# Kernel optimization log

Measured on AMD Instinct MI355X. Metric: run time of the kernel, lower is better.

## Reference

```python
import jax, jax.numpy as jnp
import numpy as np
import math

B, N, H, HEADS = 2, 4096, 256, 4
DH = H // HEADS
SCALE = math.sqrt(DH)


def setup_inputs() -> dict:
    key = jax.random.key(0)
    ks = jax.random.split(key, 8)
    h = jax.random.normal(ks[0], (B, N, H), dtype=jnp.float32)
    tau = jax.random.uniform(ks[1], (B, N), dtype=jnp.float32)  # trust scores in [0,1]
    adj_mask = jax.random.randint(ks[2], (N, N), 0, 2, dtype=jnp.int32)
    s = 0.02
    Wq = jax.random.normal(ks[3], (H, H), dtype=jnp.float32) * s
    Wk = jax.random.normal(ks[4], (H, H), dtype=jnp.float32) * s
    Wv = jax.random.normal(ks[5], (H, H), dtype=jnp.float32) * s
    Wo = jax.random.normal(ks[6], (H, H), dtype=jnp.float32) * s
    cw = jax.random.normal(ks[7], (HEADS,), dtype=jnp.float32) * s  # credibility_proj weight (num_heads,1) squeezed
    bq = jnp.zeros((H,), jnp.float32)
    bk = jnp.zeros((H,), jnp.float32)
    bv = jnp.zeros((H,), jnp.float32)
    bo = jnp.zeros((H,), jnp.float32)
    cb = jnp.zeros((HEADS,), jnp.float32)
    return {"h": h, "tau": tau, "adj_mask": adj_mask,
            "Wq": Wq, "bq": bq, "Wk": Wk, "bk": bk, "Wv": Wv, "bv": bv,
            "cw": cw, "cb": cb, "Wo": Wo, "bo": bo}


def reference(h, tau, adj_mask, Wq, bq, Wk, bk, Wv, bv, cw, cb, Wo, bo):
    # QKV projections -> (B, heads, N, head_dim)
    def proj(x, W, b):
        y = jnp.einsum('bnh,oh->bno', x, W) + b
        return y.reshape(B, N, HEADS, DH).transpose(0, 2, 1, 3)

    Q = proj(h, Wq, bq)
    K = proj(h, Wk, bk)
    V = proj(h, Wv, bv)

    scores = jnp.einsum('bhnd,bhmd->bhnm', Q, K) / SCALE  # (B,heads,N,N)
    # credibility bias: Linear(1 -> heads) applied to tau_i * tau_j
    tt = tau[:, :, None] * tau[:, None, :]                 # (B,N,N)
    cred = tt[:, None, :, :] * cw[None, :, None, None] + cb[None, :, None, None]
    scores = scores + cred
    # adjacency mask
    scores = jnp.where(adj_mask[None, None, :, :] == 0, -jnp.inf, scores)
    attention = jax.nn.softmax(scores, axis=-1)
    # dropout is identity in eval mode
    h_out = jnp.einsum('bhnm,bhmd->bhnd', attention, V)
    h_out = h_out.transpose(0, 2, 1, 3).reshape(B, N, H)
    h_out = jnp.einsum('bnh,oh->bno', h_out, Wo) + bo
    return h_out, attention.mean(axis=1)
```

## Files before the change

kernel.cpp:

```cpp
#include <hip/hip_runtime.h>

#define B_ 2
#define N_ 4096
#define H_ 256
#define HEADS_ 4
#define DH_ 64

typedef _Float16 f16;
typedef f16 f16x8 __attribute__((ext_vector_type(8)));
typedef f16 f16x4 __attribute__((ext_vector_type(4)));
typedef float f32x4 __attribute__((ext_vector_type(4)));


#define HOUT_OFF 2097152

__global__ __launch_bounds__(256) void cvt_kernel(
    const float* __restrict__ h, const float* __restrict__ Wq,
    const float* __restrict__ Wk, const float* __restrict__ Wv,
    const float* __restrict__ Wo, f16* __restrict__ ws) {
  int i = blockIdx.x * 256 + threadIdx.x;
  const int NH = 2097152;
  if (i < NH) {
    ws[i] = (f16)h[i];
  } else if (i < NH + 4 * 65536) {
    int j = i - NH;
    int sel = j >> 16;
    int k = j & 65535;
    const float* src = sel == 0 ? Wq : sel == 1 ? Wk : sel == 2 ? Wv : Wo;
    ws[i] = (f16)src[k];
  }
}

__global__ __launch_bounds__(256) void pack_adj_kernel(
    const int4* __restrict__ adj4, unsigned short* __restrict__ adjp) {
  int g = blockIdx.x * 256 + threadIdx.x;
  const int4* base = adj4 + (size_t)g * 4;
  unsigned m = 0;
#pragma unroll
  for (int t = 0; t < 4; ++t) {
    int4 v = base[t];
    m |= (unsigned)(v.x != 0) << (4 * t);
    m |= (unsigned)(v.y != 0) << (4 * t + 1);
    m |= (unsigned)(v.z != 0) << (4 * t + 2);
    m |= (unsigned)(v.w != 0) << (4 * t + 3);
  }
  adjp[g] = (unsigned short)m;
}

__global__ __launch_bounds__(256) void proj_kernel(
    const f16* __restrict__ hh, const f16* __restrict__ Wh,
    const float* __restrict__ bq, const float* __restrict__ bk,
    const float* __restrict__ bv, f16* __restrict__ Qh, f16* __restrict__ Kf,
    f16* __restrict__ Vf) {
  const int tid = threadIdx.x;
  const int lane = tid & 63, w = tid >> 6;
  const int q = lane >> 4, c = lane & 15;
  const int wsel = blockIdx.y >> 2, head = blockIdx.y & 3;
  const int m0 = blockIdx.x * 64 + w * 16;
  const f16* W = Wh + wsel * 65536;
  const int o0 = head * 64;

  f32x4 acc[4] = {};
  for (int k0 = 0; k0 < 256; k0 += 32) {
    f16x8 a = *(const f16x8*)(hh + (size_t)(m0 + c) * 256 + k0 + q * 8);
#pragma unroll
    for (int cg = 0; cg < 4; ++cg) {
      f16x8 bfr = *(const f16x8*)(W + (size_t)(o0 + cg * 16 + c) * 256 + k0 + q * 8);
      acc[cg] = __builtin_amdgcn_mfma_f32_16x16x32_f16(a, bfr, acc[cg], 0, 0, 0);
    }
  }
  const int b = m0 >> 12, n = m0 & 4095;
  const int bh2 = b * HEADS_ + head;
  if (wsel == 2) {
    const int jt = n >> 6;
    f16* vbase = Vf + (((size_t)bh2 * 64 + jt) * 8) * 512;
#pragma unroll
    for (int cg = 0; cg < 4; ++cg) {
      float bb = bv[o0 + cg * 16 + c];
#pragma unroll
      for (int r = 0; r < 4; ++r) {
        int jj = w * 16 + q * 4 + r;
        vbase[(size_t)(((jj >> 5) * 4 + cg) * 512) + ((jj >> 3) & 3) * 128 +
              c * 8 + (jj & 7)] = (f16)(acc[cg][r] + bb);
      }
    }
  } else if (wsel == 1) {
    const int t = n >> 4;
    f16* kbase = Kf + (((size_t)bh2 * 256 + t) * 2) * 512;
#pragma unroll
    for (int cg = 0; cg < 4; ++cg) {
      float bb = bk[o0 + cg * 16 + c];
      const int half = cg >> 1;
      const int qf = ((cg & 1) * 16 + c) >> 3;
      f16* kb2 = kbase + half * 512 + qf * 128 + (c & 7);
#pragma unroll
      for (int r = 0; r < 4; ++r) kb2[(q * 4 + r) * 8] = (f16)(acc[cg][r] + bb);
    }
  } else {
#pragma unroll
    for (int cg = 0; cg < 4; ++cg) {
      int dh = cg * 16 + c;
      float bb = bq[o0 + dh];
#pragma unroll
      for (int r = 0; r < 4; ++r)
        Qh[((size_t)bh2 * N_ + n + q * 4 + r) * DH_ + dh] =
            (f16)((acc[cg][r] + bb) * 0.125f);
    }
  }
}

#define TSH 80
#define PTILE (16 * TSH)

__global__ __launch_bounds__(256, 1) void attn_sum_kernel(
    const f16* __restrict__ Qh, const f16* __restrict__ Kf,
    const f16* __restrict__ Vf, const float* __restrict__ tau,
    const uint2* __restrict__ adjb, const float* __restrict__ cw,
    f16* __restrict__ Oh, float* __restrict__ rsum_ws) {
  __shared__ f16 ptile[8 * PTILE];
  __shared__ float ocomb[4][1024];
  __shared__ float lred[4][32];
  const int gid = blockIdx.x;
  const int bh = gid & 7;
  const int b = bh >> 2, h = bh & 3;
  const int i0 = (gid >> 3) * 32;
  const int tid = threadIdx.x;
  const int lane = tid & 63, jq = tid >> 6;
  const int q = lane >> 4, c = lane & 15;

  f16x8 a0[2], a1[2];
  float tau_i[2][4];
#pragma unroll
  for (int ig = 0; ig < 2; ++ig) {
    const f16* Qbase = Qh + ((size_t)bh * N_ + i0 + ig * 16 + c) * DH_;
    a0[ig] = *(const f16x8*)(Qbase + q * 8);
    a1[ig] = *(const f16x8*)(Qbase + 32 + q * 8);
#pragma unroll
    for (int r = 0; r < 4; ++r)
      tau_i[ig][r] = tau[b * N_ + i0 + ig * 16 + q * 4 + r];
  }
  const float cw_h = cw[h];
  const f16* Kfb = Kf + (size_t)bh * 262144 + lane * 8;
  const f16* Vfb = Vf + (size_t)bh * 262144 + lane * 8;
  const float* taub = tau + b * N_;
  const int jbase = jq * 1024;

  float lsum[2][4] = {};
  f32x4 oacc[2][4] = {};
  f16* myp0 = ptile + (jq * 2) * PTILE;
  f16* myp1 = myp0 + PTILE;

#pragma unroll 1
  for (int it = 0; it < 16; ++it) {
    const int j0 = jbase + it * 64;
    f16x8 kf[8];
    {
      const f16* kt = Kfb + (size_t)(j0 >> 4) * 1024;
#pragma unroll
      for (int f = 0; f < 8; ++f) kf[f] = *(const f16x8*)(kt + f * 512);
    }
    float tj[4];
#pragma unroll
    for (int cg = 0; cg < 4; ++cg) tj[cg] = taub[j0 + cg * 16 + c];

    {
      uint2 aw[4];
#pragma unroll
      for (int r = 0; r < 4; ++r)
        aw[r] = adjb[(size_t)(i0 + q * 4 + r) * 64 + (j0 >> 6)];
#pragma unroll
      for (int cg = 0; cg < 4; ++cg) {
        f32x4 s = {};
        s = __builtin_amdgcn_mfma_f32_16x16x32_f16(a0[0], kf[2 * cg], s, 0, 0, 0);
        s = __builtin_amdgcn_mfma_f32_16x16x32_f16(a1[0], kf[2 * cg + 1], s, 0, 0, 0);
        const float credj = cw_h * tj[cg];
        const unsigned shift = (cg & 1) * 16 + c;
#pragma unroll
        for (int r = 0; r < 4; ++r) {
          unsigned mword = (cg < 2) ? aw[r].x : aw[r].y;
          float e = __expf(s[r] + credj * tau_i[0][r]);
          e = ((mword >> shift) & 1) ? e : 0.f;
          lsum[0][r] += e;
          myp0[(q * 4 + r) * TSH + cg * 16 + c] = (f16)e;
        }
      }
    }
    f16x8 vf[8];
    {
      const f16* vt = Vfb + (size_t)(j0 >> 6) * 4096;
#pragma unroll
      for (int f = 0; f < 8; ++f) vf[f] = *(const f16x8*)(vt + f * 512);
    }
    {
      uint2 aw[4];
#pragma unroll
      for (int r = 0; r < 4; ++r)
        aw[r] = adjb[(size_t)(i0 + 16 + q * 4 + r) * 64 + (j0 >> 6)];
#pragma unroll
      for (int cg = 0; cg < 4; ++cg) {
        f32x4 s = {};
        s = __builtin_amdgcn_mfma_f32_16x16x32_f16(a0[1], kf[2 * cg], s, 0, 0, 0);
        s = __builtin_amdgcn_mfma_f32_16x16x32_f16(a1[1], kf[2 * cg + 1], s, 0, 0, 0);
        const float credj = cw_h * tj[cg];
        const unsigned shift = (cg & 1) * 16 + c;
#pragma unroll
        for (int r = 0; r < 4; ++r) {
          unsigned mword = (cg < 2) ? aw[r].x : aw[r].y;
          float e = __expf(s[r] + credj * tau_i[1][r]);
          e = ((mword >> shift) & 1) ? e : 0.f;
          lsum[1][r] += e;
          myp1[(q * 4 + r) * TSH + cg * 16 + c] = (f16)e;
        }
      }
    }
#pragma unroll
    for (int ig = 0; ig < 2; ++ig) {
      const f16* myp = ig ? myp1 : myp0;
#pragma unroll
      for (int ks = 0; ks < 2; ++ks) {
        f16x8 pa = *(const f16x8*)(myp + c * TSH + ks * 32 + q * 8);
#pragma unroll
        for (int cg = 0; cg < 4; ++cg)
          oacc[ig][cg] = __builtin_amdgcn_mfma_f32_16x16x32_f16(
              pa, vf[ks * 4 + cg], oacc[ig][cg], 0, 0, 0);
      }
    }
  }

#pragma unroll
  for (int ig = 0; ig < 2; ++ig) {
#pragma unroll
    for (int r = 0; r < 4; ++r) {
      float v = lsum[ig][r];
      v += __shfl_xor(v, 1);
      v += __shfl_xor(v, 2);
      v += __shfl_xor(v, 4);
      v += __shfl_xor(v, 8);
      lsum[ig][r] = v;
    }
  }
  if (c == 0) {
#pragma unroll
    for (int ig = 0; ig < 2; ++ig)
#pragma unroll
      for (int r = 0; r < 4; ++r) lred[jq][ig * 16 + q * 4 + r] = lsum[ig][r];
  }
  __syncthreads();

#pragma unroll
  for (int ig = 0; ig < 2; ++ig) {
    float linv[4];
#pragma unroll
    for (int r = 0; r < 4; ++r) {
      int row = ig * 16 + q * 4 + r;
      linv[r] = 1.0f / (lred[0][row] + lred[1][row] + lred[2][row] +
                        lred[3][row]);
    }
    if (jq == 0 && c == 0) {
#pragma unroll
      for (int r = 0; r < 4; ++r)
        rsum_ws[bh * N_ + i0 + ig * 16 + q * 4 + r] = linv[r];
    }
    if (jq != 0) {
#pragma unroll
      for (int cg = 0; cg < 4; ++cg)
#pragma unroll
        for (int r = 0; r < 4; ++r)
          ocomb[jq][(cg * 4 + r) * 64 + lane] = oacc[ig][cg][r];
    }
    __syncthreads();
    if (jq == 0) {
#pragma unroll
      for (int cg = 0; cg < 4; ++cg)
#pragma unroll
        for (int r = 0; r < 4; ++r) {
          float v = oacc[ig][cg][r];
#pragma unroll
          for (int jj = 1; jj < 4; ++jj)
            v += ocomb[jj][(cg * 4 + r) * 64 + lane];
          Oh[((size_t)(b * N_) + i0 + ig * 16 + q * 4 + r) * H_ + h * 64 +
             cg * 16 + c] = (f16)(v * linv[r]);
        }
    }
    __syncthreads();
  }
}

__global__ __launch_bounds__(256, 1) void attn_mean_kernel(
    const f16* __restrict__ Qh, const f16* __restrict__ Kf,
    const float* __restrict__ tau, const uint2* __restrict__ adjb,
    const float* __restrict__ cw, const float* __restrict__ linv_ws,
    float* __restrict__ out) {
  const int gid = blockIdx.x;
  const int b = gid & 1;
  const int jq = (gid >> 1) & 3;
  const int i0 = (gid >> 3) * 16;
  const int tid = threadIdx.x;
  const int lane = tid & 63, w = tid >> 6;
  const int q = lane >> 4, c = lane & 15;

  float li[4][4];
  float cwh[4];
#pragma unroll
  for (int h = 0; h < 4; ++h) {
    cwh[h] = cw[h];
#pragma unroll
    for (int r = 0; r < 4; ++r)
      li[h][r] = linv_ws[(b * 4 + h) * N_ + i0 + q * 4 + r] * 0.25f;
  }
  float tau_i[4];
#pragma unroll
  for (int r = 0; r < 4; ++r) tau_i[r] = tau[b * N_ + i0 + q * 4 + r];
  const float* taub = tau + b * N_;
  const f16* KfB = Kf + (size_t)(b * 4) * 262144 + lane * 8;
  const f16* QB = Qh + ((size_t)(b * 4) * N_ + i0 + c) * DH_;

  f16x8 kf2[2][8];
  f16x8 qa2[2][2];
  {
    const int j0 = jq * 1024 + w * 64;
    const f16* kt = KfB + (size_t)(j0 >> 4) * 1024;
#pragma unroll
    for (int f = 0; f < 8; ++f) kf2[0][f] = *(const f16x8*)(kt + f * 512);
    qa2[0][0] = *(const f16x8*)(QB + q * 8);
    qa2[0][1] = *(const f16x8*)(QB + 32 + q * 8);
  }

#pragma unroll 1
  for (int it = 0; it < 4; ++it) {
    const int j0 = jq * 1024 + (it * 4 + w) * 64;
    uint2 aw[4];
#pragma unroll
    for (int r = 0; r < 4; ++r)
      aw[r] = adjb[(size_t)(i0 + q * 4 + r) * 64 + (j0 >> 6)];
    float tj[4];
#pragma unroll
    for (int cg = 0; cg < 4; ++cg) tj[cg] = taub[j0 + cg * 16 + c];

    f32x4 macc[4] = {};
#pragma unroll
    for (int h = 0; h < 4; ++h) {
      const int cur = h & 1, nx = cur ^ 1;
      {
        const int hn = (h + 1) & 3;
        const int itn = (h < 3) ? it : (it < 3 ? it + 1 : it);
        const int j0n = jq * 1024 + (itn * 4 + w) * 64;
        const f16* ktn = KfB + (size_t)hn * 262144 + (size_t)(j0n >> 4) * 1024;
#pragma unroll
        for (int f = 0; f < 8; ++f) kf2[nx][f] = *(const f16x8*)(ktn + f * 512);
        const f16* qn = QB + (size_t)hn * 262144;
        qa2[nx][0] = *(const f16x8*)(qn + q * 8);
        qa2[nx][1] = *(const f16x8*)(qn + 32 + q * 8);
      }
#pragma unroll
      for (int cg = 0; cg < 4; ++cg) {
        f32x4 s = {};
        s = __builtin_amdgcn_mfma_f32_16x16x32_f16(qa2[cur][0], kf2[cur][2 * cg],
                                                   s, 0, 0, 0);
        s = __builtin_amdgcn_mfma_f32_16x16x32_f16(qa2[cur][1],
                                                   kf2[cur][2 * cg + 1], s, 0, 0, 0);
        const float credj = cwh[h] * tj[cg];
        const unsigned shift = (cg & 1) * 16 + c;
#pragma unroll
        for (int r = 0; r < 4; ++r) {
          unsigned mword = (cg < 2) ? aw[r].x : aw[r].y;
          float e = __expf(s[r] + credj * tau_i[r]);
          float lw = ((mword >> shift) & 1) ? li[h][r] : 0.f;
          macc[cg][r] += e * lw;
        }
      }
    }
#pragma unroll
    for (int cg = 0; cg < 4; ++cg)
#pragma unroll
      for (int r = 0; r < 4; ++r)
        out[((size_t)(b * N_) + i0 + q * 4 + r) * N_ + j0 + cg * 16 + c] =
            macc[cg][r];
  }
}

__global__ __launch_bounds__(256) void oproj_kernel(
    const f16* __restrict__ Oh, const f16* __restrict__ Woh,
    const float* __restrict__ bo, float* __restrict__ out) {
  const int tid = threadIdx.x, lane = tid & 63, w = tid >> 6;
  const int q = lane >> 4, c = lane & 15;
  const int m0 = blockIdx.x * 64 + w * 16;
  const int o0 = blockIdx.y * 64;
  f32x4 acc[4] = {};
  for (int k0 = 0; k0 < 256; k0 += 32) {
    f16x8 a = *(const f16x8*)(Oh + (size_t)(m0 + c) * 256 + k0 + q * 8);
#pragma unroll
    for (int cg = 0; cg < 4; ++cg) {
      f16x8 bfr = *(const f16x8*)(Woh + (size_t)(o0 + cg * 16 + c) * 256 + k0 + q * 8);
      acc[cg] = __builtin_amdgcn_mfma_f32_16x16x32_f16(a, bfr, acc[cg], 0, 0, 0);
    }
  }
#pragma unroll
  for (int cg = 0; cg < 4; ++cg) {
    float bb = bo[o0 + cg * 16 + c];
#pragma unroll
    for (int r = 0; r < 4; ++r)
      out[(size_t)(m0 + q * 4 + r) * 256 + o0 + cg * 16 + c] = acc[cg][r] + bb;
  }
}

extern "C" void kernel_launch(void* const* d_in, const int* in_sizes, int n_in,
                              void* d_out, int out_size, void* d_ws,
                              size_t ws_size, hipStream_t stream) {
  const float* h   = (const float*)d_in[0];
  const float* tau = (const float*)d_in[1];
  const int*   adj = (const int*)d_in[2];
  const float* Wq  = (const float*)d_in[3];
  const float* bq  = (const float*)d_in[4];
  const float* Wk  = (const float*)d_in[5];
  const float* bk  = (const float*)d_in[6];
  const float* Wv  = (const float*)d_in[7];
  const float* bv  = (const float*)d_in[8];
  const float* cw  = (const float*)d_in[9];
  const float* Wo  = (const float*)d_in[11];
  const float* bo  = (const float*)d_in[12];
  float* out = (float*)d_out;

  f16* ws   = (f16*)d_ws;
  f16* h_h  = ws;
  f16* W_h  = ws + 2097152;
  f16* Wo_h = W_h + 3 * 65536;
  f16* Q_h  = ws + 2359296;
  f16* K_f  = ws + 4456448;
  f16* V_f  = ws + 6553600;
  f16* O_h  = ws + 8650752;
  unsigned long long* adjb = (unsigned long long*)(ws + 10747904);
  float* rsum_ws = (float*)ws;

  pack_adj_kernel<<<dim3(4096), dim3(256), 0, stream>>>(
      (const int4*)adj, (unsigned short*)adjb);
  cvt_kernel<<<dim3(9216), dim3(256), 0, stream>>>(h, Wq, Wk, Wv, Wo, ws);
  proj_kernel<<<dim3(128, 12), dim3(256), 0, stream>>>(h_h, W_h, bq, bk, bv, Q_h,
                                                       K_f, V_f);
  attn_sum_kernel<<<dim3(1024), dim3(256), 0, stream>>>(
      Q_h, K_f, V_f, tau, (const uint2*)adjb, cw, O_h, rsum_ws);
  attn_mean_kernel<<<dim3(2048), dim3(256), 0, stream>>>(
      Q_h, K_f, tau, (const uint2*)adjb, cw, rsum_ws, out + HOUT_OFF);
  oproj_kernel<<<dim3(128, 4), dim3(256), 0, stream>>>(O_h, Wo_h, bo, out);
}
```

Baseline: 386.7 us.

## Software-pipeline K loads across iterations and store P tile as fp32 in LDS

Loads the first half of the next iteration's K fragments and tau values early so they overlap the current iteration's compute. V fragment loads are split into two halves, and the loop is unrolled by 2. The P tile in LDS is now fp32 with a 68-float stride and is converted to f16 on read. The same LDS buffer is reused for the cross-wave output combine, replacing the separate ocomb array. In exchange it raises register pressure and doubles the LDS bytes per P element, adding conversion instructions.

```diff
diff --git a/kernel.cpp b/kernel.cpp
--- a/kernel.cpp
+++ b/kernel.cpp
@@ -109,16 +109,15 @@
   }
 }
 
-#define TSH 80
-#define PTILE (16 * TSH)
+#define TS 68
+#define WTILE (16 * TS)
 
 __global__ __launch_bounds__(256, 1) void attn_sum_kernel(
     const f16* __restrict__ Qh, const f16* __restrict__ Kf,
     const f16* __restrict__ Vf, const float* __restrict__ tau,
     const uint2* __restrict__ adjb, const float* __restrict__ cw,
     f16* __restrict__ Oh, float* __restrict__ rsum_ws) {
-  __shared__ f16 ptile[8 * PTILE];
-  __shared__ float ocomb[4][1024];
+  __shared__ float lds[8 * WTILE];
   __shared__ float lred[4][32];
   const int gid = blockIdx.x;
   const int bh = gid & 7;
@@ -147,21 +146,29 @@
 
   float lsum[2][4] = {};
   f32x4 oacc[2][4] = {};
-  f16* myp0 = ptile + (jq * 2) * PTILE;
-  f16* myp1 = myp0 + PTILE;
-
-#pragma unroll 1
+  float* myp0 = lds + (jq * 2) * WTILE;
+  float* myp1 = myp0 + WTILE;
+
+  f16x8 kfA[2][4];
+  float tjA[2][4];
+  {
+    const f16* kt = Kfb + (size_t)(jbase >> 4) * 1024;
+#pragma unroll
+    for (int f = 0; f < 4; ++f) kfA[0][f] = *(const f16x8*)(kt + f * 512);
+#pragma unroll
+    for (int cg = 0; cg < 4; ++cg) tjA[0][cg] = taub[jbase + cg * 16 + c];
+  }
+
+#pragma unroll 2
   for (int it = 0; it < 16; ++it) {
+    const int cur = it & 1, nx = cur ^ 1;
     const int j0 = jbase + it * 64;
-    f16x8 kf[8];
+    f16x8 kfB[4];
     {
       const f16* kt = Kfb + (size_t)(j0 >> 4) * 1024;
 #pragma unroll
-      for (int f = 0; f < 8; ++f) kf[f] = *(const f16x8*)(kt + f * 512);
-    }
-    float tj[4];
-#pragma unroll
-    for (int cg = 0; cg < 4; ++cg) tj[cg] = taub[j0 + cg * 16 + c];
+      for (int f = 0; f < 4; ++f) kfB[f] = *(const f16x8*)(kt + (4 + f) * 512);
+    }
 
     {
       uint2 aw[4];
@@ -171,9 +178,11 @@
 #pragma unroll
       for (int cg = 0; cg < 4; ++cg) {
         f32x4 s = {};
-        s = __builtin_amdgcn_mfma_f32_16x16x32_f16(a0[0], kf[2 * cg], s, 0, 0, 0);
-        s = __builtin_amdgcn_mfma_f32_16x16x32_f16(a1[0], kf[2 * cg + 1], s, 0, 0, 0);
-        const float credj = cw_h * tj[cg];
+        f16x8 k0 = (cg < 2) ? kfA[cur][2 * cg] : kfB[2 * (cg - 2)];
+        f16x8 k1 = (cg < 2) ? kfA[cur][2 * cg + 1] : kfB[2 * (cg - 2) + 1];
+        s = __builtin_amdgcn_mfma_f32_16x16x32_f16(a0[0], k0, s, 0, 0, 0);
+        s = __builtin_amdgcn_mfma_f32_16x16x32_f16(a1[0], k1, s, 0, 0, 0);
+        const float credj = cw_h * tjA[cur][cg];
         const unsigned shift = (cg & 1) * 16 + c;
 #pragma unroll
         for (int r = 0; r < 4; ++r) {
@@ -181,16 +190,27 @@
           float e = __expf(s[r] + credj * tau_i[0][r]);
           e = ((mword >> shift) & 1) ? e : 0.f;
           lsum[0][r] += e;
-          myp0[(q * 4 + r) * TSH + cg * 16 + c] = (f16)e;
+          myp0[(q * 4 + r) * TS + cg * 16 + c] = e;
         }
       }
     }
-    f16x8 vf[8];
+
+    {
+      const int itn = (it < 15) ? it + 1 : it;
+      const int jn = jbase + itn * 64;
+      const f16* kt = Kfb + (size_t)(jn >> 4) * 1024;
+#pragma unroll
+      for (int f = 0; f < 4; ++f) kfA[nx][f] = *(const f16x8*)(kt + f * 512);
+#pragma unroll
+      for (int cg = 0; cg < 4; ++cg) tjA[nx][cg] = taub[jn + cg * 16 + c];
+    }
+    f16x8 vf0[4];
     {
       const f16* vt = Vfb + (size_t)(j0 >> 6) * 4096;
 #pragma unroll
-      for (int f = 0; f < 8; ++f) vf[f] = *(const f16x8*)(vt + f * 512);
-    }
+      for (int f = 0; f < 4; ++f) vf0[f] = *(const f16x8*)(vt + f * 512);
+    }
+
     {
       uint2 aw[4];
 #pragma unroll
@@ -199,9 +219,11 @@
 #pragma unroll
       for (int cg = 0; cg < 4; ++cg) {
         f32x4 s = {};
-        s = __builtin_amdgcn_mfma_f32_16x16x32_f16(a0[1], kf[2 * cg], s, 0, 0, 0);
-        s = __builtin_amdgcn_mfma_f32_16x16x32_f16(a1[1], kf[2 * cg + 1], s, 0, 0, 0);
-        const float credj = cw_h * tj[cg];
+        f16x8 k0 = (cg < 2) ? kfA[cur][2 * cg] : kfB[2 * (cg - 2)];
+        f16x8 k1 = (cg < 2) ? kfA[cur][2 * cg + 1] : kfB[2 * (cg - 2) + 1];
+        s = __builtin_amdgcn_mfma_f32_16x16x32_f16(a0[1], k0, s, 0, 0, 0);
+        s = __builtin_amdgcn_mfma_f32_16x16x32_f16(a1[1], k1, s, 0, 0, 0);
+        const float credj = cw_h * tjA[cur][cg];
         const unsigned shift = (cg & 1) * 16 + c;
 #pragma unroll
         for (int r = 0; r < 4; ++r) {
@@ -209,20 +231,33 @@
           float e = __expf(s[r] + credj * tau_i[1][r]);
           e = ((mword >> shift) & 1) ? e : 0.f;
           lsum[1][r] += e;
-          myp1[(q * 4 + r) * TSH + cg * 16 + c] = (f16)e;
+          myp1[(q * 4 + r) * TS + cg * 16 + c] = e;
         }
       }
     }
+    f16x8 vf1[4];
+    {
+      const f16* vt = Vfb + (size_t)(j0 >> 6) * 4096;
+#pragma unroll
+      for (int f = 0; f < 4; ++f) vf1[f] = *(const f16x8*)(vt + (4 + f) * 512);
+    }
 #pragma unroll
     for (int ig = 0; ig < 2; ++ig) {
-      const f16* myp = ig ? myp1 : myp0;
+      const float* myp = ig ? myp1 : myp0;
 #pragma unroll
       for (int ks = 0; ks < 2; ++ks) {
-        f16x8 pa = *(const f16x8*)(myp + c * TSH + ks * 32 + q * 8);
+        f32x4 plo = *(const f32x4*)(myp + c * TS + ks * 32 + q * 8);
+        f32x4 phi = *(const f32x4*)(myp + c * TS + ks * 32 + q * 8 + 4);
+        f16x8 pa;
+#pragma unroll
+        for (int t = 0; t < 4; ++t) {
+          pa[t] = (f16)plo[t];
+          pa[4 + t] = (f16)phi[t];
+        }
 #pragma unroll
         for (int cg = 0; cg < 4; ++cg)
           oacc[ig][cg] = __builtin_amdgcn_mfma_f32_16x16x32_f16(
-              pa, vf[ks * 4 + cg], oacc[ig][cg], 0, 0, 0);
+              pa, ks ? vf1[cg] : vf0[cg], oacc[ig][cg], 0, 0, 0);
       }
     }
   }
@@ -265,8 +300,7 @@
 #pragma unroll
       for (int cg = 0; cg < 4; ++cg)
 #pragma unroll
-        for (int r = 0; r < 4; ++r)
-          ocomb[jq][(cg * 4 + r) * 64 + lane] = oacc[ig][cg][r];
+        for (int r = 0; r < 4; ++r) myp0[(cg * 4 + r) * 64 + lane] = oacc[ig][cg][r];
     }
     __syncthreads();
     if (jq == 0) {
@@ -277,7 +311,7 @@
           float v = oacc[ig][cg][r];
 #pragma unroll
           for (int jj = 1; jj < 4; ++jj)
-            v += ocomb[jj][(cg * 4 + r) * 64 + lane];
+            v += lds[(jj * 2) * WTILE + (cg * 4 + r) * 64 + lane];
           Oh[((size_t)(b * N_) + i0 + ig * 16 + q * 4 + r) * H_ + h * 64 +
              cg * 16 + c] = (f16)(v * linv[r]);
         }
```

Result: slower. 397.2 us (+2.7%).

## Process 64 query rows per block in attn_sum to reuse K/V tiles

Applied to the files above, without the earlier changes.

Each attn_sum block now handles 64 query rows (four 16-row groups) instead of 32, halving the grid to 512 blocks so every K and V fragment loaded from global memory feeds twice as many MFMAs. The probability tile is staged in LDS as fp32 with a tighter stride and converted to fp16 on read-back, and the same buffer is reused for the cross-wave output reduction. V loads are split across the first two row groups to overlap with the exp work. In exchange, register pressure grows (four sets of accumulators and Q fragments), fewer blocks are available to fill the CUs, and LDS traffic per element rises.

```diff
diff --git a/kernel.cpp b/kernel.cpp
--- a/kernel.cpp
+++ b/kernel.cpp
@@ -109,29 +109,28 @@
   }
 }
 
-#define TSH 80
-#define PTILE (16 * TSH)
+#define TS 68
+#define WTILE (16 * TS)
 
 __global__ __launch_bounds__(256, 1) void attn_sum_kernel(
     const f16* __restrict__ Qh, const f16* __restrict__ Kf,
     const f16* __restrict__ Vf, const float* __restrict__ tau,
     const uint2* __restrict__ adjb, const float* __restrict__ cw,
     f16* __restrict__ Oh, float* __restrict__ rsum_ws) {
-  __shared__ f16 ptile[8 * PTILE];
-  __shared__ float ocomb[4][1024];
-  __shared__ float lred[4][32];
+  __shared__ float lds[16 * WTILE];
+  __shared__ float lred[4][64];
   const int gid = blockIdx.x;
   const int bh = gid & 7;
   const int b = bh >> 2, h = bh & 3;
-  const int i0 = (gid >> 3) * 32;
+  const int i0 = (gid >> 3) * 64;
   const int tid = threadIdx.x;
   const int lane = tid & 63, jq = tid >> 6;
   const int q = lane >> 4, c = lane & 15;
 
-  f16x8 a0[2], a1[2];
-  float tau_i[2][4];
-#pragma unroll
-  for (int ig = 0; ig < 2; ++ig) {
+  f16x8 a0[4], a1[4];
+  float tau_i[4][4];
+#pragma unroll
+  for (int ig = 0; ig < 4; ++ig) {
     const f16* Qbase = Qh + ((size_t)bh * N_ + i0 + ig * 16 + c) * DH_;
     a0[ig] = *(const f16x8*)(Qbase + q * 8);
     a1[ig] = *(const f16x8*)(Qbase + 32 + q * 8);
@@ -145,10 +144,8 @@
   const float* taub = tau + b * N_;
   const int jbase = jq * 1024;
 
-  float lsum[2][4] = {};
-  f32x4 oacc[2][4] = {};
-  f16* myp0 = ptile + (jq * 2) * PTILE;
-  f16* myp1 = myp0 + PTILE;
+  float lsum[4][4] = {};
+  f32x4 oacc[4][4] = {};
 
 #pragma unroll 1
   for (int it = 0; it < 16; ++it) {
@@ -163,62 +160,55 @@
 #pragma unroll
     for (int cg = 0; cg < 4; ++cg) tj[cg] = taub[j0 + cg * 16 + c];
 
-    {
+    f16x8 vf[8];
+#pragma unroll
+    for (int ig = 0; ig < 4; ++ig) {
+      float* myp = lds + (jq * 4 + ig) * WTILE;
       uint2 aw[4];
 #pragma unroll
       for (int r = 0; r < 4; ++r)
-        aw[r] = adjb[(size_t)(i0 + q * 4 + r) * 64 + (j0 >> 6)];
+        aw[r] = adjb[(size_t)(i0 + ig * 16 + q * 4 + r) * 64 + (j0 >> 6)];
 #pragma unroll
       for (int cg = 0; cg < 4; ++cg) {
         f32x4 s = {};
-        s = __builtin_amdgcn_mfma_f32_16x16x32_f16(a0[0], kf[2 * cg], s, 0, 0, 0);
-        s = __builtin_amdgcn_mfma_f32_16x16x32_f16(a1[0], kf[2 * cg + 1], s, 0, 0, 0);
+        s = __builtin_amdgcn_mfma_f32_16x16x32_f16(a0[ig], kf[2 * cg], s, 0, 0, 0);
+        s = __builtin_amdgcn_mfma_f32_16x16x32_f16(a1[ig], kf[2 * cg + 1], s, 0, 0, 0);
         const float credj = cw_h * tj[cg];
         const unsigned shift = (cg & 1) * 16 + c;
 #pragma unroll
         for (int r = 0; r < 4; ++r) {
           unsigned mword = (cg < 2) ? aw[r].x : aw[r].y;
-          float e = __expf(s[r] + credj * tau_i[0][r]);
+          float e = __expf(s[r] + credj * tau_i[ig][r]);
           e = ((mword >> shift) & 1) ? e : 0.f;
-          lsum[0][r] += e;
-          myp0[(q * 4 + r) * TSH + cg * 16 + c] = (f16)e;
+          lsum[ig][r] += e;
+          myp[(q * 4 + r) * TS + cg * 16 + c] = e;
         }
       }
-    }
-    f16x8 vf[8];
-    {
-      const f16* vt = Vfb + (size_t)(j0 >> 6) * 4096;
-#pragma unroll
-      for (int f = 0; f < 8; ++f) vf[f] = *(const f16x8*)(vt + f * 512);
-    }
-    {
-      uint2 aw[4];
-#pragma unroll
-      for (int r = 0; r < 4; ++r)
-        aw[r] = adjb[(size_t)(i0 + 16 + q * 4 + r) * 64 + (j0 >> 6)];
-#pragma unroll
-      for (int cg = 0; cg < 4; ++cg) {
-        f32x4 s = {};
-        s = __builtin_amdgcn_mfma_f32_16x16x32_f16(a0[1], kf[2 * cg], s, 0, 0, 0);
-        s = __builtin_amdgcn_mfma_f32_16x16x32_f16(a1[1], kf[2 * cg + 1], s, 0, 0, 0);
-        const float credj = cw_h * tj[cg];
-        const unsigned shift = (cg & 1) * 16 + c;
-#pragma unroll
-        for (int r = 0; r < 4; ++r) {
-          unsigned mword = (cg < 2) ? aw[r].x : aw[r].y;
-          float e = __expf(s[r] + credj * tau_i[1][r]);
-          e = ((mword >> shift) & 1) ? e : 0.f;
-          lsum[1][r] += e;
-          myp1[(q * 4 + r) * TSH + cg * 16 + c] = (f16)e;
+      if (ig == 0) {
+        const f16* vt = Vfb + (size_t)(j0 >> 6) * 4096;
+#pragma unroll
+        for (int f = 0; f < 4; ++f) vf[f] = *(const f16x8*)(vt + f * 512);
+      }
+      if (ig == 1) {
+        const f16* vt = Vfb + (size_t)(j0 >> 6) * 4096;
+#pragma unroll
+        for (int f = 0; f < 4; ++f) vf[4 + f] = *(const f16x8*)(vt + (4 + f) * 512);
+      }
+    }
+
+#pragma unroll
+    for (int ig = 0; ig < 4; ++ig) {
+      const float* myp = lds + (jq * 4 + ig) * WTILE;
+#pragma unroll
+      for (int ks = 0; ks < 2; ++ks) {
+        f32x4 plo = *(const f32x4*)(myp + c * TS + ks * 32 + q * 8);
+        f32x4 phi = *(const f32x4*)(myp + c * TS + ks * 32 + q * 8 + 4);
+        f16x8 pa;
+#pragma unroll
+        for (int t = 0; t < 4; ++t) {
+          pa[t] = (f16)plo[t];
+          pa[4 + t] = (f16)phi[t];
         }
-      }
-    }
-#pragma unroll
-    for (int ig = 0; ig < 2; ++ig) {
-      const f16* myp = ig ? myp1 : myp0;
-#pragma unroll
-      for (int ks = 0; ks < 2; ++ks) {
-        f16x8 pa = *(const f16x8*)(myp + c * TSH + ks * 32 + q * 8);
 #pragma unroll
         for (int cg = 0; cg < 4; ++cg)
           oacc[ig][cg] = __builtin_amdgcn_mfma_f32_16x16x32_f16(
@@ -228,7 +218,7 @@
   }
 
 #pragma unroll
-  for (int ig = 0; ig < 2; ++ig) {
+  for (int ig = 0; ig < 4; ++ig) {
 #pragma unroll
     for (int r = 0; r < 4; ++r) {
       float v = lsum[ig][r];
@@ -241,14 +231,14 @@
   }
   if (c == 0) {
 #pragma unroll
-    for (int ig = 0; ig < 2; ++ig)
+    for (int ig = 0; ig < 4; ++ig)
 #pragma unroll
       for (int r = 0; r < 4; ++r) lred[jq][ig * 16 + q * 4 + r] = lsum[ig][r];
   }
   __syncthreads();
 
 #pragma unroll
-  for (int ig = 0; ig < 2; ++ig) {
+  for (int ig = 0; ig < 4; ++ig) {
     float linv[4];
 #pragma unroll
     for (int r = 0; r < 4; ++r) {
@@ -266,7 +256,7 @@
       for (int cg = 0; cg < 4; ++cg)
 #pragma unroll
         for (int r = 0; r < 4; ++r)
-          ocomb[jq][(cg * 4 + r) * 64 + lane] = oacc[ig][cg][r];
+          lds[(jq * 4) * WTILE + (cg * 4 + r) * 64 + lane] = oacc[ig][cg][r];
     }
     __syncthreads();
     if (jq == 0) {
@@ -277,7 +267,7 @@
           float v = oacc[ig][cg][r];
 #pragma unroll
           for (int jj = 1; jj < 4; ++jj)
-            v += ocomb[jj][(cg * 4 + r) * 64 + lane];
+            v += lds[(jj * 4) * WTILE + (cg * 4 + r) * 64 + lane];
           Oh[((size_t)(b * N_) + i0 + ig * 16 + q * 4 + r) * H_ + h * 64 +
              cg * 16 + c] = (f16)(v * linv[r]);
         }
@@ -437,7 +427,7 @@
   cvt_kernel<<<dim3(9216), dim3(256), 0, stream>>>(h, Wq, Wk, Wv, Wo, ws);
   proj_kernel<<<dim3(128, 12), dim3(256), 0, stream>>>(h_h, W_h, bq, bk, bv, Q_h,
                                                        K_f, V_f);
-  attn_sum_kernel<<<dim3(1024), dim3(256), 0, stream>>>(
+  attn_sum_kernel<<<dim3(512), dim3(256), 0, stream>>>(
       Q_h, K_f, V_f, tau, (const uint2*)adjb, cw, O_h, rsum_ws);
   attn_mean_kernel<<<dim3(2048), dim3(256), 0, stream>>>(
       Q_h, K_f, tau, (const uint2*)adjb, cw, rsum_ws, out + HOUT_OFF);
```

New measurement: 415.5 us. 1.07x slower.
